# Performance work log

Measured on AMD Instinct MI355X. Metric: run time of the kernel, lower is better.

## Reference

```python
import jax, jax.numpy as jnp
import numpy as np

QUERY_DIM = 192
KEY_DIM = 64
DIM_OUT = 128
C = QUERY_DIM + KEY_DIM  # 256
N = 10000
E = 320000
M = 5000


def setup_inputs() -> dict:
    key = jax.random.key(0)
    ks = jax.random.split(key, 16)
    s = 1.0 / np.sqrt(C)
    inp = {
        "query": jax.random.normal(ks[0], (N, QUERY_DIM), jnp.float32),
        "key_idx": jax.random.randint(ks[1], (N,), 0, KEY_DIM),
        "edge_index": jax.random.randint(ks[2], (2, E), 0, N),
        "mask_idx": jnp.sort(jax.random.randint(ks[3], (M,), 0, N)),
        "Wq": jax.random.normal(ks[4], (C, C), jnp.float32) * s,
        "bq": jnp.zeros((C,), jnp.float32),
        "Wk": jax.random.normal(ks[5], (C, C), jnp.float32) * s,
        "bk": jnp.zeros((C,), jnp.float32),
        "Wv": jax.random.normal(ks[6], (C, C), jnp.float32) * s,
        "bv": jnp.zeros((C,), jnp.float32),
        "Ws": jax.random.normal(ks[7], (C, C), jnp.float32) * s,
        "bs": jnp.zeros((C,), jnp.float32),
        "Wo": jax.random.normal(ks[8], (KEY_DIM, DIM_OUT), jnp.float32) * (1.0 / np.sqrt(KEY_DIM)),
        "bo": jnp.zeros((DIM_OUT,), jnp.float32),
    }
    return inp


def reference(query, key_idx, edge_index, mask_idx, Wq, bq, Wk, bk, Wv, bv, Ws, bs, Wo, bo):
    # node features: [N, C] = concat(query, one_hot(key))
    x = jnp.concatenate([query, jax.nn.one_hot(key_idx, KEY_DIM, dtype=query.dtype)], axis=1)
    src, dst = edge_index[0], edge_index[1]  # messages flow src -> dst
    # node-level projections (dense GEMMs), then edge gather
    q_n = x @ Wq + bq
    k_n = x @ Wk + bk
    v_n = x @ Wv + bv
    q = q_n[dst]  # [E, C]
    k = k_n[src]
    v = v_n[src]
    score = jnp.sum(q * k, axis=-1) / jnp.sqrt(jnp.asarray(C, x.dtype))  # [E]
    # per-destination softmax over incoming edges
    m = jax.ops.segment_max(score, dst, num_segments=N)  # [N]
    m = jnp.where(jnp.isfinite(m), m, 0.0)
    e = jnp.exp(score - m[dst])
    denom = jax.ops.segment_sum(e, dst, num_segments=N)
    alpha = e / (denom[dst] + 1e-16)
    # scatter-aggregate weighted values + root/skip connection
    agg = jax.ops.segment_sum(alpha[:, None] * v, dst, num_segments=N)  # [N, C]
    out = agg + (x @ Ws + bs)
    h = jax.nn.relu(out[mask_idx])  # [M, C]
    h = h[:, QUERY_DIM:]  # [M, KEY_DIM]
    return h @ Wo + bo  # [M, DIM_OUT]
```

## Files before the change

kernel.cpp:

```cpp
#include <hip/hip_runtime.h>

#define QDIM 192
#define KDIM 64
#define CDIM 256
#define DOUT 128
#define CAP 128
#define NEG_INF __int_as_float(0xFF800000)
#define LDP 200

typedef _Float16 hf2 __attribute__((ext_vector_type(2)));
typedef _Float16 half4 __attribute__((ext_vector_type(4)));
typedef _Float16 half8 __attribute__((ext_vector_type(8)));
typedef float floatx4 __attribute__((ext_vector_type(4)));

#if defined(__has_builtin)
#if __has_builtin(__builtin_amdgcn_fdot2)
#define HAVE_FDOT2 1
#endif
#endif

__device__ __forceinline__ hf2 bc_h2(unsigned u) { return __builtin_bit_cast(hf2, u); }

__device__ __forceinline__ float dot2acc(hf2 a, hf2 b, float c) {
#ifdef HAVE_FDOT2
    return __builtin_amdgcn_fdot2(a, b, c, false);
#else
    return c + (float)a[0] * (float)b[0] + (float)a[1] * (float)b[1];
#endif
}

__global__ __launch_bounds__(256) void prep_kernel(
        const float* __restrict__ query, _Float16* __restrict__ Qh,
        int* __restrict__ deg, int qchunks, int N) {
    int t = blockIdx.x * blockDim.x + threadIdx.x;
    if (t < qchunks) {
        float4 v = ((const float4*)query)[t];
        half4 h = { (_Float16)v.x, (_Float16)v.y, (_Float16)v.z, (_Float16)v.w };
        ((half4*)Qh)[t] = h;
        return;
    }
    t -= qchunks;
    if (t < N) deg[t] = (int)0x80000000;
}

__global__ __launch_bounds__(256) void gemm_nodes(
        const _Float16* __restrict__ Qh, const int* __restrict__ key_idx,
        const float* Wq, const float* bq, const float* Wk, const float* bk,
        const float* Wv, const float* bv, const float* Ws, const float* bs,
        const int* __restrict__ mask, int M, int* __restrict__ deg,
        _Float16* __restrict__ Qbuf, _Float16* __restrict__ Kbuf,
        _Float16* __restrict__ Vbuf, float* __restrict__ Sbuf, int N) {
    __shared__ __align__(16) _Float16 As[64 * LDP];
    __shared__ __align__(16) _Float16 Bs[64 * LDP];
    int bm = blockIdx.x * 64;
    int bn = blockIdx.y * 64;
    int tid = threadIdx.x;

    int gid = (blockIdx.y * gridDim.x + blockIdx.x) * 256 + tid;
    if (gid < M) deg[mask[gid]] = 0;

    const float* Wb; const float* bvec; int wc0;
    if (bn < 256)      { Wb = Wq; bvec = bq; wc0 = bn; }
    else if (bn < 512) { Wb = Wk; bvec = bk; wc0 = bn - 256; }
    else if (bn < 576) { Wb = Wv; bvec = bv; wc0 = QDIM + (bn - 512); }
    else               { Wb = Ws; bvec = bs; wc0 = QDIM + (bn - 576); }

    #pragma unroll
    for (int it = 0; it < 6; it++) {
        int idx = tid + it * 256;
        int r = idx / 24, q4 = idx % 24;
        int gr = bm + r;
        uint4 va = make_uint4(0u, 0u, 0u, 0u);
        if (gr < N) va = ((const uint4*)(Qh + (size_t)gr * QDIM))[q4];
        *((uint4*)&As[r * LDP + q4 * 8]) = va;
    }
    {
        int c = tid & 63, r0 = tid >> 6;
        #pragma unroll
        for (int it = 0; it < 6; it++) {
            int kg = r0 + it * 4;
            float f[8];
            #pragma unroll
            for (int j = 0; j < 8; j++)
                f[j] = Wb[(size_t)(kg * 8 + j) * CDIM + wc0 + c];
            half8 h8 = { (_Float16)f[0], (_Float16)f[1], (_Float16)f[2], (_Float16)f[3],
                         (_Float16)f[4], (_Float16)f[5], (_Float16)f[6], (_Float16)f[7] };
            *((half8*)&Bs[c * LDP + kg * 8]) = h8;
        }
    }
    __syncthreads();

    int w = tid >> 6, l = tid & 63;
    int lrow = l & 15, quad = l >> 4;
    floatx4 acc[4] = {{0.f,0.f,0.f,0.f},{0.f,0.f,0.f,0.f},{0.f,0.f,0.f,0.f},{0.f,0.f,0.f,0.f}};

    const _Float16* arow = &As[(w * 16 + lrow) * LDP + quad * 8];
    #pragma unroll
    for (int ks = 0; ks < 6; ks++) {
        half8 af = *(const half8*)(arow + ks * 32);
        #pragma unroll
        for (int nt = 0; nt < 4; nt++) {
            half8 bf = *(const half8*)(&Bs[(nt * 16 + lrow) * LDP + quad * 8 + ks * 32]);
            acc[nt] = __builtin_amdgcn_mfma_f32_16x16x32_f16(af, bf, acc[nt], 0, 0, 0);
        }
    }

    int ki[4];
    #pragma unroll
    for (int reg = 0; reg < 4; reg++) {
        int gr = bm + w * 16 + quad * 4 + reg;
        ki[reg] = (gr < N) ? key_idx[gr] : 0;
    }
    #pragma unroll
    for (int nt = 0; nt < 4; nt++) {
        int gc = bn + nt * 16 + lrow;
        int wc = wc0 + nt * 16 + lrow;
        float bias = bvec[wc];
        #pragma unroll
        for (int reg = 0; reg < 4; reg++) {
            int gr = bm + w * 16 + quad * 4 + reg;
            if (gr < N) {
                float v = acc[nt][reg] + Wb[(size_t)(QDIM + ki[reg]) * CDIM + wc] + bias;
                if (gc < 256)      Qbuf[(size_t)gr * 256 + gc] = (_Float16)v;
                else if (gc < 512) Kbuf[(size_t)gr * 256 + (gc - 256)] = (_Float16)v;
                else if (gc < 576) Vbuf[(size_t)gr * KDIM + (gc - 512)] = (_Float16)v;
                else               Sbuf[(size_t)gr * KDIM + (gc - 576)] = v;
            }
        }
    }
}

__global__ __launch_bounds__(256) void scatter_kernel(
        const int* __restrict__ src, const int* __restrict__ dst,
        int* __restrict__ deg, int* __restrict__ adj, int E) {
    int e = blockIdx.x * blockDim.x + threadIdx.x;
    if (e < E) {
        int d = dst[e];
        int slot = atomicAdd(&deg[d], 1);
        if ((unsigned)slot < CAP) adj[d * CAP + slot] = src[e];
    }
}

__global__ __launch_bounds__(256) void attend_out(
        const _Float16* __restrict__ Qbuf, const _Float16* __restrict__ Kbuf,
        const _Float16* __restrict__ Vbuf, const float* __restrict__ Sbuf,
        const int* __restrict__ deg, const int* __restrict__ adj,
        const int* __restrict__ mask, const float* __restrict__ Wo,
        const float* __restrict__ bo, float* __restrict__ out, int M) {
    int w = threadIdx.x >> 6, lane = threadIdx.x & 63;
    int r = blockIdx.x * 4 + w;
    if (r >= M) return;
    int node = mask[r];
    if (r > 0 && mask[r - 1] == node) return;
    int l = lane & 15, g = lane >> 4;

    const uint4* qp = (const uint4*)(Qbuf + (size_t)node * 256 + l * 16);
    uint4 qa = qp[0], qb = qp[1];
    hf2 qh[8] = { bc_h2(qa.x), bc_h2(qa.y), bc_h2(qa.z), bc_h2(qa.w),
                  bc_h2(qb.x), bc_h2(qb.y), bc_h2(qb.z), bc_h2(qb.w) };

    int dn = min(deg[node], CAP);
    const int* arow = adj + (size_t)node * CAP;

    float m = NEG_INF, dsum = 0.f;
    float a0 = 0.f, a1 = 0.f, a2 = 0.f, a3 = 0.f;
    for (int i = g; i < dn; i += 4) {
        int s = arow[i];
        const uint4* kp = (const uint4*)(Kbuf + (size_t)s * 256 + l * 16);
        uint4 ka = kp[0], kb = kp[1];
        float d = 0.f;
        d = dot2acc(bc_h2(ka.x), qh[0], d);
        d = dot2acc(bc_h2(ka.y), qh[1], d);
        d = dot2acc(bc_h2(ka.z), qh[2], d);
        d = dot2acc(bc_h2(ka.w), qh[3], d);
        d = dot2acc(bc_h2(kb.x), qh[4], d);
        d = dot2acc(bc_h2(kb.y), qh[5], d);
        d = dot2acc(bc_h2(kb.z), qh[6], d);
        d = dot2acc(bc_h2(kb.w), qh[7], d);
        d += __shfl_xor(d, 1, 64);
        d += __shfl_xor(d, 2, 64);
        d += __shfl_xor(d, 4, 64);
        d += __shfl_xor(d, 8, 64);
        float sc = d * 0.0625f;
        float m_new = fmaxf(m, sc);
        float scale = __expf(m - m_new);
        float p = __expf(sc - m_new);
        dsum = dsum * scale + p;
        uint2 vv = *(const uint2*)(Vbuf + (size_t)s * KDIM + l * 4);
        hf2 v01 = bc_h2(vv.x), v23 = bc_h2(vv.y);
        a0 = a0 * scale + p * (float)v01[0];
        a1 = a1 * scale + p * (float)v01[1];
        a2 = a2 * scale + p * (float)v23[0];
        a3 = a3 * scale + p * (float)v23[1];
        m = m_new;
    }

    float Mx = fmaxf(m, __shfl_xor(m, 16, 64));
    Mx = fmaxf(Mx, __shfl_xor(Mx, 32, 64));
    float wgt = (m == NEG_INF) ? 0.f : __expf(m - Mx);
    float ds = dsum * wgt;
    ds += __shfl_xor(ds, 16, 64);
    ds += __shfl_xor(ds, 32, 64);
    a0 *= wgt; a1 *= wgt; a2 *= wgt; a3 *= wgt;
    a0 += __shfl_xor(a0, 16, 64); a0 += __shfl_xor(a0, 32, 64);
    a1 += __shfl_xor(a1, 16, 64); a1 += __shfl_xor(a1, 32, 64);
    a2 += __shfl_xor(a2, 16, 64); a2 += __shfl_xor(a2, 32, 64);
    a3 += __shfl_xor(a3, 16, 64); a3 += __shfl_xor(a3, 32, 64);
    float inv = 1.f / (ds + 1e-16f);

    float4 s4 = *((const float4*)(Sbuf + (size_t)node * KDIM + l * 4));
    float h0 = fmaxf(a0 * inv + s4.x, 0.f);
    float h1 = fmaxf(a1 * inv + s4.y, 0.f);
    float h2 = fmaxf(a2 * inv + s4.z, 0.f);
    float h3 = fmaxf(a3 * inv + s4.w, 0.f);

    float o0 = bo[lane], o1 = bo[lane + 64];
    #pragma unroll
    for (int c = 0; c < KDIM; c++) {
        float hc = (c & 3) == 0 ? h0 : (c & 3) == 1 ? h1 : (c & 3) == 2 ? h2 : h3;
        float hv = __shfl(hc, c >> 2, 64);
        o0 += hv * Wo[c * DOUT + lane];
        o1 += hv * Wo[c * DOUT + 64 + lane];
    }
    int rr = r;
    do {
        out[(size_t)rr * DOUT + lane] = o0;
        out[(size_t)rr * DOUT + 64 + lane] = o1;
        rr++;
    } while (rr < M && mask[rr] == node);
}

extern "C" void kernel_launch(void* const* d_in, const int* in_sizes, int n_in,
                              void* d_out, int out_size, void* d_ws, size_t ws_size,
                              hipStream_t stream) {
    const float* query    = (const float*)d_in[0];
    const int* key_idx    = (const int*)d_in[1];
    const int* edge_index = (const int*)d_in[2];
    const int* mask_idx   = (const int*)d_in[3];
    const float* Wq = (const float*)d_in[4];
    const float* bq = (const float*)d_in[5];
    const float* Wk = (const float*)d_in[6];
    const float* bk = (const float*)d_in[7];
    const float* Wv = (const float*)d_in[8];
    const float* bv = (const float*)d_in[9];
    const float* Ws = (const float*)d_in[10];
    const float* bs = (const float*)d_in[11];
    const float* Wo = (const float*)d_in[12];
    const float* bo = (const float*)d_in[13];

    int N = in_sizes[0] / QDIM;
    int E = in_sizes[2] / 2;
    int M = in_sizes[3];
    const int* esrc = edge_index;
    const int* edst = edge_index + E;

    char* wsb = (char*)d_ws;
    size_t off = 0;
    auto alloc = [&](size_t nbytes) { char* p = wsb + off; off += (nbytes + 15) & ~15ull; return p; };
    _Float16* Qh   = (_Float16*)alloc((size_t)N * QDIM * 2);
    _Float16* Qbuf = (_Float16*)alloc((size_t)N * 256 * 2);
    _Float16* Kbuf = (_Float16*)alloc((size_t)N * 256 * 2);
    _Float16* Vbuf = (_Float16*)alloc((size_t)N * KDIM * 2);
    float* Sbuf    = (float*)alloc((size_t)N * KDIM * 4);
    int*   deg     = (int*)alloc((size_t)N * 4);
    int*   adj     = (int*)alloc((size_t)N * CAP * 4);

    int qchunks = N * QDIM / 4;
    prep_kernel<<<(qchunks + N + 255) / 256, 256, 0, stream>>>(query, Qh, deg, qchunks, N);

    dim3 ggrid((N + 63) / 64, 10);
    gemm_nodes<<<ggrid, 256, 0, stream>>>(Qh, key_idx, Wq, bq, Wk, bk, Wv, bv,
                                          Ws, bs, mask_idx, M, deg,
                                          Qbuf, Kbuf, Vbuf, Sbuf, N);

    scatter_kernel<<<(E + 255) / 256, 256, 0, stream>>>(esrc, edst, deg, adj, E);

    attend_out<<<(M + 3) / 4, 256, 0, stream>>>(Qbuf, Kbuf, Vbuf, Sbuf, deg, adj,
                                                mask_idx, Wo, bo, (float*)d_out, M);
}
```

Baseline: 148.4 us.

## Fuse edge scatter and query conversion into node GEMM, reuse A tile

Folds the fp32-to-fp16 query conversion and the edge-bucket scatter into the node projection GEMM. The scatter runs as a grid-stride loop at the start of each block. Each block now computes two 64-column output tiles from one converted A tile, halving the grid's y dimension. The degree array is zeroed with a memset rather than sentinel-initialised for unmasked nodes, which removes two kernel launches and the Qh round-trip. In exchange, adjacency entries are now written for every destination node, not only masked ones, and the atomics share the GEMM blocks' time.

```diff
diff --git a/kernel.cpp b/kernel.cpp
--- a/kernel.cpp
+++ b/kernel.cpp
@@ -29,81 +29,42 @@
 #endif
 }
 
-__global__ __launch_bounds__(256) void prep_kernel(
-        const float* __restrict__ query, _Float16* __restrict__ Qh,
-        int* __restrict__ deg, int qchunks, int N) {
-    int t = blockIdx.x * blockDim.x + threadIdx.x;
-    if (t < qchunks) {
-        float4 v = ((const float4*)query)[t];
-        half4 h = { (_Float16)v.x, (_Float16)v.y, (_Float16)v.z, (_Float16)v.w };
-        ((half4*)Qh)[t] = h;
-        return;
-    }
-    t -= qchunks;
-    if (t < N) deg[t] = (int)0x80000000;
-}
-
-__global__ __launch_bounds__(256) void gemm_nodes(
-        const _Float16* __restrict__ Qh, const int* __restrict__ key_idx,
+__global__ __launch_bounds__(256) void gemm_scatter(
+        const float* __restrict__ query, const int* __restrict__ key_idx,
         const float* Wq, const float* bq, const float* Wk, const float* bk,
         const float* Wv, const float* bv, const float* Ws, const float* bs,
-        const int* __restrict__ mask, int M, int* __restrict__ deg,
+        const int* __restrict__ esrc, const int* __restrict__ edst,
+        int* __restrict__ deg, int* __restrict__ adj, int E,
         _Float16* __restrict__ Qbuf, _Float16* __restrict__ Kbuf,
         _Float16* __restrict__ Vbuf, float* __restrict__ Sbuf, int N) {
     __shared__ __align__(16) _Float16 As[64 * LDP];
     __shared__ __align__(16) _Float16 Bs[64 * LDP];
     int bm = blockIdx.x * 64;
-    int bn = blockIdx.y * 64;
     int tid = threadIdx.x;
 
-    int gid = (blockIdx.y * gridDim.x + blockIdx.x) * 256 + tid;
-    if (gid < M) deg[mask[gid]] = 0;
-
-    const float* Wb; const float* bvec; int wc0;
-    if (bn < 256)      { Wb = Wq; bvec = bq; wc0 = bn; }
-    else if (bn < 512) { Wb = Wk; bvec = bk; wc0 = bn - 256; }
-    else if (bn < 576) { Wb = Wv; bvec = bv; wc0 = QDIM + (bn - 512); }
-    else               { Wb = Ws; bvec = bs; wc0 = QDIM + (bn - 576); }
+    {
+        int total = gridDim.x * gridDim.y * 256;
+        int gid = (blockIdx.y * gridDim.x + blockIdx.x) * 256 + tid;
+        for (int e = gid; e < E; e += total) {
+            int d = edst[e];
+            int slot = atomicAdd(&deg[d], 1);
+            if (slot < CAP) adj[d * CAP + slot] = esrc[e];
+        }
+    }
 
     #pragma unroll
-    for (int it = 0; it < 6; it++) {
+    for (int it = 0; it < 12; it++) {
         int idx = tid + it * 256;
-        int r = idx / 24, q4 = idx % 24;
+        int r = idx / 48, f4 = idx % 48;
         int gr = bm + r;
-        uint4 va = make_uint4(0u, 0u, 0u, 0u);
-        if (gr < N) va = ((const uint4*)(Qh + (size_t)gr * QDIM))[q4];
-        *((uint4*)&As[r * LDP + q4 * 8]) = va;
-    }
-    {
-        int c = tid & 63, r0 = tid >> 6;
-        #pragma unroll
-        for (int it = 0; it < 6; it++) {
-            int kg = r0 + it * 4;
-            float f[8];
-            #pragma unroll
-            for (int j = 0; j < 8; j++)
-                f[j] = Wb[(size_t)(kg * 8 + j) * CDIM + wc0 + c];
-            half8 h8 = { (_Float16)f[0], (_Float16)f[1], (_Float16)f[2], (_Float16)f[3],
-                         (_Float16)f[4], (_Float16)f[5], (_Float16)f[6], (_Float16)f[7] };
-            *((half8*)&Bs[c * LDP + kg * 8]) = h8;
-        }
-    }
-    __syncthreads();
+        float4 va = make_float4(0.f, 0.f, 0.f, 0.f);
+        if (gr < N) va = ((const float4*)(query + (size_t)gr * QDIM))[f4];
+        half4 h = { (_Float16)va.x, (_Float16)va.y, (_Float16)va.z, (_Float16)va.w };
+        *((half4*)&As[r * LDP + f4 * 4]) = h;
+    }
 
     int w = tid >> 6, l = tid & 63;
     int lrow = l & 15, quad = l >> 4;
-    floatx4 acc[4] = {{0.f,0.f,0.f,0.f},{0.f,0.f,0.f,0.f},{0.f,0.f,0.f,0.f},{0.f,0.f,0.f,0.f}};
-
-    const _Float16* arow = &As[(w * 16 + lrow) * LDP + quad * 8];
-    #pragma unroll
-    for (int ks = 0; ks < 6; ks++) {
-        half8 af = *(const half8*)(arow + ks * 32);
-        #pragma unroll
-        for (int nt = 0; nt < 4; nt++) {
-            half8 bf = *(const half8*)(&Bs[(nt * 16 + lrow) * LDP + quad * 8 + ks * 32]);
-            acc[nt] = __builtin_amdgcn_mfma_f32_16x16x32_f16(af, bf, acc[nt], 0, 0, 0);
-        }
-    }
 
     int ki[4];
     #pragma unroll
@@ -111,33 +72,61 @@
         int gr = bm + w * 16 + quad * 4 + reg;
         ki[reg] = (gr < N) ? key_idx[gr] : 0;
     }
-    #pragma unroll
-    for (int nt = 0; nt < 4; nt++) {
-        int gc = bn + nt * 16 + lrow;
-        int wc = wc0 + nt * 16 + lrow;
-        float bias = bvec[wc];
+
+    for (int t = 0; t < 2; t++) {
+        int bn = blockIdx.y * 128 + t * 64;
+        const float* Wb; const float* bvec; int wc0;
+        if (bn < 256)      { Wb = Wq; bvec = bq; wc0 = bn; }
+        else if (bn < 512) { Wb = Wk; bvec = bk; wc0 = bn - 256; }
+        else if (bn < 576) { Wb = Wv; bvec = bv; wc0 = QDIM + (bn - 512); }
+        else               { Wb = Ws; bvec = bs; wc0 = QDIM + (bn - 576); }
+
+        if (t > 0) __syncthreads();
+        {
+            int c = tid & 63, r0 = tid >> 6;
+            #pragma unroll
+            for (int it = 0; it < 6; it++) {
+                int kg = r0 + it * 4;
+                float f[8];
+                #pragma unroll
+                for (int j = 0; j < 8; j++)
+                    f[j] = Wb[(size_t)(kg * 8 + j) * CDIM + wc0 + c];
+                half8 h8 = { (_Float16)f[0], (_Float16)f[1], (_Float16)f[2], (_Float16)f[3],
+                             (_Float16)f[4], (_Float16)f[5], (_Float16)f[6], (_Float16)f[7] };
+                *((half8*)&Bs[c * LDP + kg * 8]) = h8;
+            }
+        }
+        __syncthreads();
+
+        floatx4 acc[4] = {{0.f,0.f,0.f,0.f},{0.f,0.f,0.f,0.f},{0.f,0.f,0.f,0.f},{0.f,0.f,0.f,0.f}};
+        const _Float16* arow = &As[(w * 16 + lrow) * LDP + quad * 8];
         #pragma unroll
-        for (int reg = 0; reg < 4; reg++) {
-            int gr = bm + w * 16 + quad * 4 + reg;
-            if (gr < N) {
-                float v = acc[nt][reg] + Wb[(size_t)(QDIM + ki[reg]) * CDIM + wc] + bias;
-                if (gc < 256)      Qbuf[(size_t)gr * 256 + gc] = (_Float16)v;
-                else if (gc < 512) Kbuf[(size_t)gr * 256 + (gc - 256)] = (_Float16)v;
-                else if (gc < 576) Vbuf[(size_t)gr * KDIM + (gc - 512)] = (_Float16)v;
-                else               Sbuf[(size_t)gr * KDIM + (gc - 576)] = v;
+        for (int ks = 0; ks < 6; ks++) {
+            half8 af = *(const half8*)(arow + ks * 32);
+            #pragma unroll
+            for (int nt = 0; nt < 4; nt++) {
+                half8 bf = *(const half8*)(&Bs[(nt * 16 + lrow) * LDP + quad * 8 + ks * 32]);
+                acc[nt] = __builtin_amdgcn_mfma_f32_16x16x32_f16(af, bf, acc[nt], 0, 0, 0);
             }
         }
-    }
-}
-
-__global__ __launch_bounds__(256) void scatter_kernel(
-        const int* __restrict__ src, const int* __restrict__ dst,
-        int* __restrict__ deg, int* __restrict__ adj, int E) {
-    int e = blockIdx.x * blockDim.x + threadIdx.x;
-    if (e < E) {
-        int d = dst[e];
-        int slot = atomicAdd(&deg[d], 1);
-        if ((unsigned)slot < CAP) adj[d * CAP + slot] = src[e];
+
+        #pragma unroll
+        for (int nt = 0; nt < 4; nt++) {
+            int gc = bn + nt * 16 + lrow;
+            int wc = wc0 + nt * 16 + lrow;
+            float bias = bvec[wc];
+            #pragma unroll
+            for (int reg = 0; reg < 4; reg++) {
+                int gr = bm + w * 16 + quad * 4 + reg;
+                if (gr < N) {
+                    float v = acc[nt][reg] + Wb[(size_t)(QDIM + ki[reg]) * CDIM + wc] + bias;
+                    if (gc < 256)      Qbuf[(size_t)gr * 256 + gc] = (_Float16)v;
+                    else if (gc < 512) Kbuf[(size_t)gr * 256 + (gc - 256)] = (_Float16)v;
+                    else if (gc < 576) Vbuf[(size_t)gr * KDIM + (gc - 512)] = (_Float16)v;
+                    else               Sbuf[(size_t)gr * KDIM + (gc - 576)] = v;
+                }
+            }
+        }
     }
 }
 
@@ -257,7 +246,6 @@
     char* wsb = (char*)d_ws;
     size_t off = 0;
     auto alloc = [&](size_t nbytes) { char* p = wsb + off; off += (nbytes + 15) & ~15ull; return p; };
-    _Float16* Qh   = (_Float16*)alloc((size_t)N * QDIM * 2);
     _Float16* Qbuf = (_Float16*)alloc((size_t)N * 256 * 2);
     _Float16* Kbuf = (_Float16*)alloc((size_t)N * 256 * 2);
     _Float16* Vbuf = (_Float16*)alloc((size_t)N * KDIM * 2);
@@ -265,15 +253,12 @@
     int*   deg     = (int*)alloc((size_t)N * 4);
     int*   adj     = (int*)alloc((size_t)N * CAP * 4);
 
-    int qchunks = N * QDIM / 4;
-    prep_kernel<<<(qchunks + N + 255) / 256, 256, 0, stream>>>(query, Qh, deg, qchunks, N);
-
-    dim3 ggrid((N + 63) / 64, 10);
-    gemm_nodes<<<ggrid, 256, 0, stream>>>(Qh, key_idx, Wq, bq, Wk, bk, Wv, bv,
-                                          Ws, bs, mask_idx, M, deg,
-                                          Qbuf, Kbuf, Vbuf, Sbuf, N);
-
-    scatter_kernel<<<(E + 255) / 256, 256, 0, stream>>>(esrc, edst, deg, adj, E);
+    hipMemsetAsync(deg, 0, (size_t)N * 4, stream);
+
+    dim3 ggrid((N + 63) / 64, 5);
+    gemm_scatter<<<ggrid, 256, 0, stream>>>(query, key_idx, Wq, bq, Wk, bk, Wv, bv,
+                                            Ws, bs, esrc, edst, deg, adj, E,
+                                            Qbuf, Kbuf, Vbuf, Sbuf, N);
 
     attend_out<<<(M + 3) / 4, 256, 0, stream>>>(Qbuf, Kbuf, Vbuf, Sbuf, deg, adj,
                                                 mask_idx, Wo, bo, (float*)d_out, M);
```

Result: slower. 151.6 us (+2.1%).
